# Kernel optimization log

Measured on AMD Instinct MI355X. Metric: run time of the kernel, lower is better.

Reference implementation:

```python
import jax, jax.numpy as jnp
import numpy as np

T, B, H, L2, C = 1132, 128, 13, 100, 10  # seq, batch, hidden, total layers (2x50), classes


def setup_inputs() -> dict:
    key = jax.random.key(0)
    ks = jax.random.split(key, 7)
    s = 1.0 / np.sqrt(H)  # torch LSTM/Linear default init scale
    return {
        "input": jax.random.normal(ks[0], (B, T, H), jnp.float32),
        "w_ih": jax.random.uniform(ks[1], (L2, 4 * H, H), jnp.float32, -s, s),
        "w_hh": jax.random.uniform(ks[2], (L2, 4 * H, H), jnp.float32, -s, s),
        "b_ih": jax.random.uniform(ks[3], (L2, 4 * H), jnp.float32, -s, s),
        "b_hh": jax.random.uniform(ks[4], (L2, 4 * H), jnp.float32, -s, s),
        "w_lin": jax.random.uniform(ks[5], (C, T * H), jnp.float32, -1.0 / np.sqrt(T * H), 1.0 / np.sqrt(T * H)),
        "b_lin": jax.random.uniform(ks[6], (C,), jnp.float32, -1.0 / np.sqrt(T * H), 1.0 / np.sqrt(T * H)),
    }


def _lstm_stack(x, w_ih, w_hh, b_ih, b_hh):
    # x: [T, B, H]; weights stacked over layers: [L, 4H, H], biases [L, 4H]
    def layer(x, params):
        Wih, Whh, bih, bhh = params
        # input contribution for all timesteps at once (one big GEMM)
        pre = jnp.einsum('tbf,gf->tbg', x, Wih) + bih + bhh  # [T, B, 4H]

        def step(carry, p):
            h, c = carry
            g = p + h @ Whh.T  # [B, 4H]
            i, f, gg, o = jnp.split(g, 4, axis=-1)  # torch gate order: i,f,g,o
            c = jax.nn.sigmoid(f) * c + jax.nn.sigmoid(i) * jnp.tanh(gg)
            h = jax.nn.sigmoid(o) * jnp.tanh(c)
            return (h, c), h

        h0 = jnp.zeros((x.shape[1], Whh.shape[1]), x.dtype)
        _, hs = jax.lax.scan(step, (h0, h0), pre)
        return hs, None

    x, _ = jax.lax.scan(layer, x, (w_ih, w_hh, b_ih, b_hh))
    return x


def reference(input, w_ih, w_hh, b_ih, b_hh, w_lin, b_lin):
    x = jnp.transpose(input, (1, 0, 2))  # [T, B, H] (time-major for scan)
    x = _lstm_stack(x, w_ih, w_hh, b_ih, b_hh)
    x = jnp.transpose(x, (1, 0, 2)).reshape(input.shape[0], -1)  # [B, T*H]
    logits = x @ w_lin.T + b_lin
    return jax.nn.softmax(logits, axis=1)
```

## Files before the change

kernel.cpp:

```cpp
#include <hip/hip_runtime.h>
#include <stdint.h>

#define T_SEQ  1132
#define BATCH  128
#define HID    13
#define G4     52
#define NLAYER 100
#define NPIPE  8
#define LPW    4
#define NWGP   25
#define NTHR   384
#define CH     4
#define NCH    283
#define RCL    4
#define RC     8
#define NCLS   10
#define FEAT   (T_SEQ*HID)

#define CHUNK_U32 (CH*256)
#define FLAG_BYTES 65536
#define RING_U32_PER_WG ((size_t)RC * CHUNK_U32)
#define RING_BYTES ((size_t)(NPIPE*NWGP) * RING_U32_PER_WG * 4)

typedef float  f32x4 __attribute__((ext_vector_type(4)));
typedef __fp16 f16x4 __attribute__((ext_vector_type(4)));
typedef unsigned int u32x4 __attribute__((ext_vector_type(4)));

struct HL { f16x4 h; f16x4 l; };

__device__ __forceinline__ float sigm(float x) {
  return __builtin_amdgcn_rcpf(1.0f + __expf(-x));
}
__device__ __forceinline__ float tanh_(float x) {
  return 1.0f - 2.0f * __builtin_amdgcn_rcpf(1.0f + __expf(2.0f * x));
}
__device__ __forceinline__ void f16split(float x, __fp16& hi, __fp16& lo) {
  hi = (__fp16)x;
  lo = (__fp16)(x - (float)hi);
}

__device__ __forceinline__ void lspin_ge(int* p, int need) {
  int v = __hip_atomic_load(p, __ATOMIC_ACQUIRE, __HIP_MEMORY_SCOPE_WORKGROUP);
  while (v < need) {
    __builtin_amdgcn_s_sleep(1);
    v = __hip_atomic_load(p, __ATOMIC_ACQUIRE, __HIP_MEMORY_SCOPE_WORKGROUP);
  }
}
__device__ __forceinline__ void gspin_ge(int* p, int need) {
  int v = __hip_atomic_load(p, __ATOMIC_RELAXED, __HIP_MEMORY_SCOPE_AGENT);
  while (v < need) {
    __builtin_amdgcn_s_sleep(1);
    v = __hip_atomic_load(p, __ATOMIC_RELAXED, __HIP_MEMORY_SCOPE_AGENT);
  }
}

__global__ __launch_bounds__(NTHR) void lstm_pipeline(
    const float* __restrict__ xin,
    const float* __restrict__ w_ih,
    const float* __restrict__ w_hh,
    const float* __restrict__ b_ih,
    const float* __restrict__ b_hh,
    int*      flags,
    uint32_t* ring,
    float*    act)
{
  const int wg   = blockIdx.x;
  const int pp   = wg / NWGP;
  const int wgi  = wg - pp * NWGP;
  const int tid  = threadIdx.x;
  const int lane = tid & 63;
  const int nt   = tid >> 6;
  const int quad = lane >> 4;
  const int b15  = lane & 15;
  const bool lastWG = (wgi == NWGP - 1);

  __shared__ __align__(16) uint32_t sXP[LPW][RCL][CH][256];
  __shared__ __align__(16) uint32_t sOutR[RCL][CH][256];
  __shared__ int sProg[LPW];
  __shared__ int sCons[LPW];
  __shared__ int sProgOut;
  __shared__ int sConsOut;

  int* flReadySelf = flags + ((pp * NWGP + wgi) * 2 + 0) * 16;
  int* flProgSelf  = flags + ((pp * NWGP + wgi) * 2 + 1) * 16;
  int* flReadyPrev = (wgi > 0) ? flags + ((pp * NWGP + wgi - 1) * 2 + 0) * 16 : flags;
  int* flProgNext  = (!lastWG) ? flags + ((pp * NWGP + wgi + 1) * 2 + 1) * 16 : flags;

  if (lane == 0) {
    if (nt == LPW + 1)
      __hip_atomic_store(flReadySelf, 0, __ATOMIC_RELAXED, __HIP_MEMORY_SCOPE_AGENT);
    if (nt == LPW)
      __hip_atomic_store(flProgSelf, 0, __ATOMIC_RELAXED, __HIP_MEMORY_SCOPE_AGENT);
  }
  if (tid < LPW) { sProg[tid] = 0; sCons[tid] = 0; }
  if (tid == 0) { sProgOut = 0; sConsOut = 0; }
  __syncthreads();

  if (nt < LPW) {
    const int l = wgi * LPW + nt;
    const bool lastL = (l == NLAYER - 1);

    f16x4 Axh[4], Axl[4], Ahh[4], Ahl[4];
    f32x4 biasv[4];
    #pragma unroll
    for (int mt = 0; mt < 4; ++mt) {
      #pragma unroll
      for (int jj = 0; jj < 4; ++jj) {
        int k = quad * 4 + jj;
        float wx = 0.f, wh = 0.f;
        if (b15 < HID && k < HID) {
          int g = mt * HID + b15;
          wx = w_ih[(size_t)(l * G4 + g) * HID + k];
          wh = w_hh[(size_t)(l * G4 + g) * HID + k];
        }
        __fp16 hi, lo;
        f16split(wx, hi, lo); Axh[mt][jj] = hi; Axl[mt][jj] = lo;
        f16split(wh, hi, lo); Ahh[mt][jj] = hi; Ahl[mt][jj] = lo;
      }
      #pragma unroll
      for (int r = 0; r < 4; ++r) {
        int jt = quad * 4 + r;
        biasv[mt][r] = (jt < HID)
            ? (b_ih[l * G4 + mt * HID + jt] + b_hh[l * G4 + mt * HID + jt]) : 0.f;
      }
    }

    f16x4 Bhh = (f16x4)0, Bhl = (f16x4)0;
    float cst[4] = {0.f, 0.f, 0.f, 0.f};

    #pragma unroll 1
    for (int ci = 0; ci < NCH; ++ci) {
      const int slot = ci & (RCL - 1);

      lspin_ge(&sProg[nt], ci + 1);
      if (ci + 1 - RCL > 0) {
        if (nt < LPW - 1) lspin_ge(&sCons[nt + 1], ci + 1 - RCL);
        else              lspin_ge(&sConsOut,       ci + 1 - RCL);
      }

      f32x4 ax[CH][4];
      #pragma unroll
      for (int s = 0; s < CH; ++s) {
        u32x4 bx = *(const u32x4*)&sXP[nt][slot][s][lane * 4];
        HL z = __builtin_bit_cast(HL, bx);
        #pragma unroll
        for (int mt = 0; mt < 4; ++mt) {
          f32x4 a = biasv[mt];
          a = __builtin_amdgcn_mfma_f32_16x16x16f16(Axh[mt], z.h, a, 0, 0, 0);
          a = __builtin_amdgcn_mfma_f32_16x16x16f16(Axl[mt], z.h, a, 0, 0, 0);
          a = __builtin_amdgcn_mfma_f32_16x16x16f16(Axh[mt], z.l, a, 0, 0, 0);
          ax[s][mt] = a;
        }
      }
      if (lane == 0)
        __hip_atomic_store(&sCons[nt], ci + 1, __ATOMIC_RELEASE, __HIP_MEMORY_SCOPE_WORKGROUP);

      #pragma unroll
      for (int s = 0; s < CH; ++s) {
        f32x4 acc[4];
        #pragma unroll
        for (int mt = 0; mt < 4; ++mt) {
          f32x4 a = ax[s][mt];
          a = __builtin_amdgcn_mfma_f32_16x16x16f16(Ahh[mt], Bhh, a, 0, 0, 0);
          a = __builtin_amdgcn_mfma_f32_16x16x16f16(Ahl[mt], Bhh, a, 0, 0, 0);
          a = __builtin_amdgcn_mfma_f32_16x16x16f16(Ahh[mt], Bhl, a, 0, 0, 0);
          acc[mt] = a;
        }
        float hnv[4];
        #pragma unroll
        for (int r = 0; r < 4; ++r) {
          float gi = acc[0][r], gf = acc[1][r], gg = acc[2][r], go = acc[3][r];
          float c = sigm(gf) * cst[r] + sigm(gi) * tanh_(gg);
          cst[r] = c;
          float h = sigm(go) * tanh_(c);
          hnv[r] = h;
          __fp16 hi, lo; f16split(h, hi, lo);
          Bhh[r] = hi; Bhl[r] = lo;
        }
        if (nt < LPW - 1) {
          HL o; o.h = Bhh; o.l = Bhl;
          *(u32x4*)&sXP[nt + 1][slot][s][lane * 4] = __builtin_bit_cast(u32x4, o);
        } else if (!lastL) {
          HL o; o.h = Bhh; o.l = Bhl;
          *(u32x4*)&sOutR[slot][s][lane * 4] = __builtin_bit_cast(u32x4, o);
        } else {
          u32x4 w;
          #pragma unroll
          for (int r = 0; r < 4; ++r) w[r] = __float_as_uint(hnv[r]);
          *(u32x4*)&sOutR[slot][s][lane * 4] = w;
        }
      }

      if (lane == 0) {
        if (nt < LPW - 1)
          __hip_atomic_store(&sProg[nt + 1], ci + 1, __ATOMIC_RELEASE, __HIP_MEMORY_SCOPE_WORKGROUP);
        else
          __hip_atomic_store(&sProgOut, ci + 1, __ATOMIC_RELEASE, __HIP_MEMORY_SCOPE_WORKGROUP);
      }
    }
  } else if (nt == LPW) {
    const uint32_t* ringprev = ring + (size_t)(pp * NWGP + wgi - 1) * RING_U32_PER_WG;
    const size_t    xrow     = (size_t)(pp * 16 + b15) * (T_SEQ * HID);

    #pragma unroll 1
    for (int cin = 0; cin < NCH; ++cin) {
      const int slot = cin & (RCL - 1);
      if (cin + 1 - RCL > 0) lspin_ge(&sCons[0], cin + 1 - RCL);

      if (wgi > 0) {
        gspin_ge(flReadyPrev, cin + 1);
        const uint32_t* src = ringprev + (size_t)(cin & (RC - 1)) * CHUNK_U32;
        uint32_t v[CH][4];
        #pragma unroll
        for (int s = 0; s < CH; ++s)
          #pragma unroll
          for (int w = 0; w < 4; ++w)
            v[s][w] = __hip_atomic_load(&src[s * 256 + lane * 4 + w],
                                        __ATOMIC_RELAXED, __HIP_MEMORY_SCOPE_AGENT);
        #pragma unroll
        for (int s = 0; s < CH; ++s) {
          u32x4 q = { v[s][0], v[s][1], v[s][2], v[s][3] };
          *(u32x4*)&sXP[0][slot][s][lane * 4] = q;
        }
        asm volatile("s_waitcnt vmcnt(0)" ::: "memory");
        if (lane == 0)
          __hip_atomic_store(flProgSelf, cin + 1, __ATOMIC_RELAXED, __HIP_MEMORY_SCOPE_AGENT);
      } else {
        const int t0 = cin * CH;
        #pragma unroll
        for (int s = 0; s < CH; ++s) {
          HL o;
          #pragma unroll
          for (int jj = 0; jj < 4; ++jj) {
            int k = quad * 4 + jj;
            float v = (k < HID) ? xin[xrow + (size_t)(t0 + s) * HID + k] : 0.f;
            __fp16 hi, lo; f16split(v, hi, lo);
            o.h[jj] = hi; o.l[jj] = lo;
          }
          *(u32x4*)&sXP[0][slot][s][lane * 4] = __builtin_bit_cast(u32x4, o);
        }
      }
      if (lane == 0)
        __hip_atomic_store(&sProg[0], cin + 1, __ATOMIC_RELEASE, __HIP_MEMORY_SCOPE_WORKGROUP);
    }
  } else {
    uint32_t* ringmine = ring + (size_t)(pp * NWGP + wgi) * RING_U32_PER_WG;

    #pragma unroll 1
    for (int cout = 0; cout < NCH; ++cout) {
      const int slot = cout & (RCL - 1);
      lspin_ge(&sProgOut, cout + 1);

      if (!lastWG) {
        if (cout + 1 - RC > 0) gspin_ge(flProgNext, cout + 1 - RC);
        uint32_t* dst = ringmine + (size_t)(cout & (RC - 1)) * CHUNK_U32;
        #pragma unroll
        for (int s = 0; s < CH; ++s) {
          u32x4 v = *(const u32x4*)&sOutR[slot][s][lane * 4];
          #pragma unroll
          for (int w = 0; w < 4; ++w)
            __hip_atomic_store(&dst[s * 256 + lane * 4 + w], v[w],
                               __ATOMIC_RELAXED, __HIP_MEMORY_SCOPE_AGENT);
        }
        asm volatile("s_waitcnt vmcnt(0)" ::: "memory");
        if (lane == 0) {
          __hip_atomic_store(flReadySelf, cout + 1, __ATOMIC_RELAXED, __HIP_MEMORY_SCOPE_AGENT);
          __hip_atomic_store(&sConsOut, cout + 1, __ATOMIC_RELEASE, __HIP_MEMORY_SCOPE_WORKGROUP);
        }
      } else {
        const int t0 = cout * CH;
        #pragma unroll
        for (int s = 0; s < CH; ++s) {
          u32x4 v = *(const u32x4*)&sOutR[slot][s][lane * 4];
          float* dst = act + (size_t)(t0 + s) * (BATCH * HID)
                     + (size_t)(pp * 16 + b15) * HID + quad * 4;
          #pragma unroll
          for (int r = 0; r < 4; ++r)
            if (quad * 4 + r < HID) dst[r] = __uint_as_float(v[r]);
        }
        if (lane == 0)
          __hip_atomic_store(&sConsOut, cout + 1, __ATOMIC_RELEASE, __HIP_MEMORY_SCOPE_WORKGROUP);
      }
    }
  }
}

__global__ __launch_bounds__(256) void linear_softmax(
    const float* __restrict__ act,
    const float* __restrict__ w_lin,
    const float* __restrict__ b_lin,
    float* __restrict__ out)
{
  const int b   = blockIdx.x;
  const int tid = threadIdx.x;
  float accv[NCLS];
  #pragma unroll
  for (int c = 0; c < NCLS; ++c) accv[c] = 0.f;

  for (int i = tid; i < FEAT; i += 256) {
    int t = i / HID; int jj = i - t * HID;
    float a = act[(size_t)t * (BATCH * HID) + b * HID + jj];
    #pragma unroll
    for (int c = 0; c < NCLS; ++c)
      accv[c] += a * w_lin[(size_t)c * FEAT + i];
  }

  __shared__ float red[NCLS][256];
  #pragma unroll
  for (int c = 0; c < NCLS; ++c) red[c][tid] = accv[c];
  __syncthreads();
  for (int off = 128; off > 0; off >>= 1) {
    if (tid < off) {
      #pragma unroll
      for (int c = 0; c < NCLS; ++c) red[c][tid] += red[c][tid + off];
    }
    __syncthreads();
  }
  if (tid == 0) {
    float lg[NCLS]; float mx = -1e30f;
    #pragma unroll
    for (int c = 0; c < NCLS; ++c) { lg[c] = red[c][0] + b_lin[c]; mx = fmaxf(mx, lg[c]); }
    float sum = 0.f;
    #pragma unroll
    for (int c = 0; c < NCLS; ++c) { lg[c] = __expf(lg[c] - mx); sum += lg[c]; }
    float inv = 1.0f / sum;
    #pragma unroll
    for (int c = 0; c < NCLS; ++c) out[b * NCLS + c] = lg[c] * inv;
  }
}

extern "C" void kernel_launch(void* const* d_in, const int* in_sizes, int n_in,
                              void* d_out, int out_size, void* d_ws, size_t ws_size,
                              hipStream_t stream) {
  const float* xin  = (const float*)d_in[0];
  const float* wih  = (const float*)d_in[1];
  const float* whh  = (const float*)d_in[2];
  const float* bih  = (const float*)d_in[3];
  const float* bhh  = (const float*)d_in[4];
  const float* wlin = (const float*)d_in[5];
  const float* blin = (const float*)d_in[6];

  char*     ws    = (char*)d_ws;
  int*      flags = (int*)ws;
  uint32_t* ring  = (uint32_t*)(ws + FLAG_BYTES);
  float*    act   = (float*)(ws + FLAG_BYTES + RING_BYTES);

  lstm_pipeline<<<NPIPE * NWGP, NTHR, 0, stream>>>(xin, wih, whh, bih, bhh, flags, ring, act);
  linear_softmax<<<BATCH, 256, 0, stream>>>(act, wlin, blin, (float*)d_out);
}
```

Before: 983.5 us.

## Prefetch next ring chunk, coalesce ring layout, release LDS slot before global stores

The input-loader wave now issues the global ring loads for chunk ci+1 before writing chunk ci into LDS, overlapping cross-workgroup fetch latency with local handoff. Ring accesses switch from lane*4+w to w*64+lane so each per-word atomic load and store is coalesced across the wave. The output wave signals the LDS slot free before writing to global memory, and flag polling caches the last seen value to skip redundant atomic loads. The consumed-progress flag is published one chunk later, which shrinks the effective ring depth and slightly delays upstream producers.

```diff
diff --git a/kernel.cpp b/kernel.cpp
--- a/kernel.cpp
+++ b/kernel.cpp
@@ -39,6 +39,8 @@
   lo = (__fp16)(x - (float)hi);
 }
 
+#define VMCNT0() asm volatile("s_waitcnt vmcnt(0)" ::: "memory")
+
 __device__ __forceinline__ void lspin_ge(int* p, int need) {
   int v = __hip_atomic_load(p, __ATOMIC_ACQUIRE, __HIP_MEMORY_SCOPE_WORKGROUP);
   while (v < need) {
@@ -46,12 +48,12 @@
     v = __hip_atomic_load(p, __ATOMIC_ACQUIRE, __HIP_MEMORY_SCOPE_WORKGROUP);
   }
 }
-__device__ __forceinline__ void gspin_ge(int* p, int need) {
-  int v = __hip_atomic_load(p, __ATOMIC_RELAXED, __HIP_MEMORY_SCOPE_AGENT);
-  while (v < need) {
-    __builtin_amdgcn_s_sleep(1);
-    v = __hip_atomic_load(p, __ATOMIC_RELAXED, __HIP_MEMORY_SCOPE_AGENT);
-  }
+__device__ __forceinline__ int gwait_ge(int* p, int need, int cached) {
+  while (cached < need) {
+    cached = __hip_atomic_load(p, __ATOMIC_RELAXED, __HIP_MEMORY_SCOPE_AGENT);
+    if (cached < need) __builtin_amdgcn_s_sleep(1);
+  }
+  return cached;
 }
 
 __global__ __launch_bounds__(NTHR) void lstm_pipeline(
@@ -199,33 +201,56 @@
       }
     }
   } else if (nt == LPW) {
-    const uint32_t* ringprev = ring + (size_t)(pp * NWGP + wgi - 1) * RING_U32_PER_WG;
-    const size_t    xrow     = (size_t)(pp * 16 + b15) * (T_SEQ * HID);
-
-    #pragma unroll 1
-    for (int cin = 0; cin < NCH; ++cin) {
-      const int slot = cin & (RCL - 1);
-      if (cin + 1 - RCL > 0) lspin_ge(&sCons[0], cin + 1 - RCL);
-
-      if (wgi > 0) {
-        gspin_ge(flReadyPrev, cin + 1);
-        const uint32_t* src = ringprev + (size_t)(cin & (RC - 1)) * CHUNK_U32;
-        uint32_t v[CH][4];
+    if (wgi > 0) {
+      const uint32_t* ringprev = ring + (size_t)(pp * NWGP + wgi - 1) * RING_U32_PER_WG;
+      u32x4 nxt[CH];
+      int cPrev = gwait_ge(flReadyPrev, 1, 0);
+      {
+        const uint32_t* src = ringprev;
         #pragma unroll
         for (int s = 0; s < CH; ++s)
           #pragma unroll
           for (int w = 0; w < 4; ++w)
-            v[s][w] = __hip_atomic_load(&src[s * 256 + lane * 4 + w],
-                                        __ATOMIC_RELAXED, __HIP_MEMORY_SCOPE_AGENT);
-        #pragma unroll
-        for (int s = 0; s < CH; ++s) {
-          u32x4 q = { v[s][0], v[s][1], v[s][2], v[s][3] };
-          *(u32x4*)&sXP[0][slot][s][lane * 4] = q;
-        }
-        asm volatile("s_waitcnt vmcnt(0)" ::: "memory");
-        if (lane == 0)
-          __hip_atomic_store(flProgSelf, cin + 1, __ATOMIC_RELAXED, __HIP_MEMORY_SCOPE_AGENT);
-      } else {
+            nxt[s][w] = __hip_atomic_load(&src[s * 256 + w * 64 + lane],
+                                          __ATOMIC_RELAXED, __HIP_MEMORY_SCOPE_AGENT);
+      }
+      #pragma unroll 1
+      for (int ci = 0; ci < NCH; ++ci) {
+        u32x4 cur[CH];
+        #pragma unroll
+        for (int s = 0; s < CH; ++s) cur[s] = nxt[s];
+
+        if (ci + 1 < NCH) {
+          cPrev = gwait_ge(flReadyPrev, ci + 2, cPrev);
+          const uint32_t* src = ringprev + (size_t)((ci + 1) & (RC - 1)) * CHUNK_U32;
+          #pragma unroll
+          for (int s = 0; s < CH; ++s)
+            #pragma unroll
+            for (int w = 0; w < 4; ++w)
+              nxt[s][w] = __hip_atomic_load(&src[s * 256 + w * 64 + lane],
+                                            __ATOMIC_RELAXED, __HIP_MEMORY_SCOPE_AGENT);
+        }
+
+        if (ci + 1 - RCL > 0) lspin_ge(&sCons[0], ci + 1 - RCL);
+        const int slot = ci & (RCL - 1);
+        #pragma unroll
+        for (int s = 0; s < CH; ++s)
+          *(u32x4*)&sXP[0][slot][s][lane * 4] = cur[s];
+        if (lane == 0) {
+          __hip_atomic_store(&sProg[0], ci + 1, __ATOMIC_RELEASE, __HIP_MEMORY_SCOPE_WORKGROUP);
+          if (ci > 0)
+            __hip_atomic_store(flProgSelf, ci, __ATOMIC_RELAXED, __HIP_MEMORY_SCOPE_AGENT);
+        }
+      }
+      VMCNT0();
+      if (lane == 0)
+        __hip_atomic_store(flProgSelf, NCH, __ATOMIC_RELAXED, __HIP_MEMORY_SCOPE_AGENT);
+    } else {
+      const size_t xrow = (size_t)(pp * 16 + b15) * (T_SEQ * HID);
+      #pragma unroll 1
+      for (int cin = 0; cin < NCH; ++cin) {
+        const int slot = cin & (RCL - 1);
+        if (cin + 1 - RCL > 0) lspin_ge(&sCons[0], cin + 1 - RCL);
         const int t0 = cin * CH;
         #pragma unroll
         for (int s = 0; s < CH; ++s) {
@@ -239,35 +264,40 @@
           }
           *(u32x4*)&sXP[0][slot][s][lane * 4] = __builtin_bit_cast(u32x4, o);
         }
-      }
-      if (lane == 0)
-        __hip_atomic_store(&sProg[0], cin + 1, __ATOMIC_RELEASE, __HIP_MEMORY_SCOPE_WORKGROUP);
+        if (lane == 0)
+          __hip_atomic_store(&sProg[0], cin + 1, __ATOMIC_RELEASE, __HIP_MEMORY_SCOPE_WORKGROUP);
+      }
     }
   } else {
-    uint32_t* ringmine = ring + (size_t)(pp * NWGP + wgi) * RING_U32_PER_WG;
-
-    #pragma unroll 1
-    for (int cout = 0; cout < NCH; ++cout) {
-      const int slot = cout & (RCL - 1);
-      lspin_ge(&sProgOut, cout + 1);
-
-      if (!lastWG) {
-        if (cout + 1 - RC > 0) gspin_ge(flProgNext, cout + 1 - RC);
+    if (!lastWG) {
+      uint32_t* ringmine = ring + (size_t)(pp * NWGP + wgi) * RING_U32_PER_WG;
+      int cNext = 0;
+      #pragma unroll 1
+      for (int cout = 0; cout < NCH; ++cout) {
+        lspin_ge(&sProgOut, cout + 1);
+        if (cout + 1 - RC > 0) cNext = gwait_ge(flProgNext, cout + 1 - RC, cNext);
+        const int slot = cout & (RCL - 1);
+        u32x4 v[CH];
+        #pragma unroll
+        for (int s = 0; s < CH; ++s) v[s] = *(const u32x4*)&sOutR[slot][s][lane * 4];
+        if (lane == 0)
+          __hip_atomic_store(&sConsOut, cout + 1, __ATOMIC_RELEASE, __HIP_MEMORY_SCOPE_WORKGROUP);
         uint32_t* dst = ringmine + (size_t)(cout & (RC - 1)) * CHUNK_U32;
         #pragma unroll
-        for (int s = 0; s < CH; ++s) {
-          u32x4 v = *(const u32x4*)&sOutR[slot][s][lane * 4];
+        for (int s = 0; s < CH; ++s)
           #pragma unroll
           for (int w = 0; w < 4; ++w)
-            __hip_atomic_store(&dst[s * 256 + lane * 4 + w], v[w],
+            __hip_atomic_store(&dst[s * 256 + w * 64 + lane], v[s][w],
                                __ATOMIC_RELAXED, __HIP_MEMORY_SCOPE_AGENT);
-        }
-        asm volatile("s_waitcnt vmcnt(0)" ::: "memory");
-        if (lane == 0) {
+        VMCNT0();
+        if (lane == 0)
           __hip_atomic_store(flReadySelf, cout + 1, __ATOMIC_RELAXED, __HIP_MEMORY_SCOPE_AGENT);
-          __hip_atomic_store(&sConsOut, cout + 1, __ATOMIC_RELEASE, __HIP_MEMORY_SCOPE_WORKGROUP);
-        }
-      } else {
+      }
+    } else {
+      #pragma unroll 1
+      for (int cout = 0; cout < NCH; ++cout) {
+        lspin_ge(&sProgOut, cout + 1);
+        const int slot = cout & (RCL - 1);
         const int t0 = cout * CH;
         #pragma unroll
         for (int s = 0; s < CH; ++s) {
```

New measurement: 1.019 ms. 1.04x slower.
